# Optimization experiments

Hardware: AMD Instinct MI355X
Metric: run time of the kernel (lower is better)

## Reference

```python
import jax, jax.numpy as jnp
import numpy as np

N = 4096  # flattened_input_shape


def setup_inputs() -> dict:
    key = jax.random.key(0)
    ks = jax.random.split(key, 5)
    eps = 0.1
    center = jax.random.normal(ks[0], (1, N), dtype=jnp.float32)
    lb0 = center - eps  # initial interval lower bounds [1, N]
    ub0 = center + eps  # initial interval upper bounds [1, N]
    W1 = jax.random.normal(ks[1], (N, N), dtype=jnp.float32) / np.float32(np.sqrt(N))
    b1 = jax.random.normal(ks[2], (1, N), dtype=jnp.float32)
    W2 = jax.random.normal(ks[3], (N, N), dtype=jnp.float32) / np.float32(np.sqrt(N))
    b2 = jax.random.normal(ks[4], (1, N), dtype=jnp.float32)
    raw_alpha = jnp.ones((N,), dtype=jnp.float32)  # nn.Parameter init
    return {"raw_alpha": raw_alpha, "lb0": lb0, "ub0": ub0,
            "W1": W1, "b1": b1, "W2": W2, "b2": b2}


def _pos(x):
    return jnp.where(x > 0, x, jnp.zeros_like(x))


def _neg(x):
    return jnp.where(x < 0, x, jnp.zeros_like(x))


def _forward(raw_alpha, lb0, ub0, W1, b1, W2, b2):
    # ---- previous.backsubstitution(): compose affine2 over affine1 ----
    clslope, clintercept = W2, b2
    cuslope, cuintercept = W2, b2
    clp, cln = _pos(clslope), _neg(clslope)
    cup, cun = _pos(cuslope), _neg(cuslope)
    clintercept = b1 @ clp.T + b1 @ cln.T + clintercept  # [1, N]
    cuintercept = b1 @ cup.T + b1 @ cun.T + cuintercept  # [1, N]
    clslope = clp @ W1 + cln @ W1  # [N, N]
    cuslope = cup @ W1 + cun @ W1  # [N, N]
    # ---- certifier against initial interval bounds ----
    lbounds = lb0 @ _pos(clslope).T + ub0 @ _neg(clslope).T + clintercept  # [1, N]
    ubounds = ub0 @ _pos(cuslope).T + lb0 @ _neg(cuslope).T + cuintercept  # [1, N]
    # ---- DeepPolyReLU transformer ----
    alpha = jax.nn.sigmoid(raw_alpha)  # [N]
    lb = lbounds.reshape(-1)
    ub = ubounds.reshape(-1)
    denom = ub - lb
    # ub/(ub-lb) with NaN (0/0) replaced by 0, grad-safe
    relu_slope = jnp.where(denom == 0, 0.0, ub / jnp.where(denom == 0, 1.0, denom))  # [N]
    relu_intercept = (1.0 - relu_slope)[None, :] * ubounds  # [1, N]
    below = ub <= 0
    above = lb >= 0
    crossing = ~(below | above)
    base = jnp.where(above, 1.0, 0.0)  # [N]
    uslope = jnp.where(crossing, relu_slope, base)
    uintercept = jnp.where(crossing[None, :], relu_intercept, jnp.zeros((1, N), dtype=ubounds.dtype))
    lslope_v1 = jnp.where(crossing, 0.0, base)
    lslope_v2 = jnp.where(crossing, 1.0, base)
    lslope = alpha * lslope_v1 + (1.0 - alpha) * lslope_v2  # [N]
    lintercept = jnp.zeros((1, N), dtype=lbounds.dtype)
    return jnp.diag(lslope), lintercept, jnp.diag(uslope), uintercept


def reference(raw_alpha, lb0, ub0, W1, b1, W2, b2):
    return _forward(raw_alpha, lb0, ub0, W1, b1, W2, b2)
```

## Files before the change

### kernel.cpp

```cpp
#include <hip/hip_runtime.h>
#include <stdint.h>

#define N 4096
#define BM 128
#define BN 128
#define BK 128

#define TILE_BYTES 524288
#define KT_BYTES   16384

#define QSCALE 256.0f
#define INV_QQ (1.0f / 65536.0f)

typedef int v8i __attribute__((ext_vector_type(8)));
typedef float f32x16 __attribute__((ext_vector_type(16)));

union V8 { v8i v; uint4 h[2]; };

__device__ __forceinline__ void gload16(const unsigned char* g, unsigned char* l) {
  __builtin_amdgcn_global_load_lds(
      (const __attribute__((address_space(1))) unsigned int*)g,
      (__attribute__((address_space(3))) unsigned int*)l, 16, 0, 0);
}

__device__ __forceinline__ int pack4_fp8(float a, float b, float c, float d) {
  int r = __builtin_amdgcn_cvt_pk_fp8_f32(a, b, 0, false);
  r = __builtin_amdgcn_cvt_pk_fp8_f32(c, d, r, true);
  return r;
}

__global__ __launch_bounds__(256) void prep_w1(const float* __restrict__ W1,
                                               const float* __restrict__ lb0,
                                               const float* __restrict__ ub0,
                                               unsigned char* __restrict__ W1T,
                                               float* __restrict__ tvec) {
  __shared__ float tile[64 * 65];
  __shared__ float tdot[64];
  const int t = threadIdx.x;
  const int j0 = blockIdx.x * 64, k0 = blockIdx.y * 64;
  if (t < 64) tdot[t] = 0.f;
  __syncthreads();
#pragma unroll
  for (int s = 0; s < 4; ++s) {
    int ck = s * 256 + t;
    int row = ck >> 4;
    int col = (ck & 15) * 4;
    float4 v = *(const float4*)(W1 + (size_t)(k0 + row) * N + j0 + col);
    float4 l = *(const float4*)(lb0 + j0 + col);
    float4 u = *(const float4*)(ub0 + j0 + col);
    float part = v.x * 0.5f * (l.x + u.x) + v.y * 0.5f * (l.y + u.y)
               + v.z * 0.5f * (l.z + u.z) + v.w * 0.5f * (l.w + u.w);
    atomicAdd(&tdot[row], part);
    float* d = &tile[row * 65 + col];
    d[0] = v.x; d[1] = v.y; d[2] = v.z; d[3] = v.w;
  }
  __syncthreads();
  if (t < 64) atomicAdd(&tvec[k0 + t], tdot[t]);
  int jl = t >> 2, ch = (t & 3) * 16;
  float f[16];
#pragma unroll
  for (int m = 0; m < 16; ++m) f[m] = tile[(ch + m) * 65 + jl] * QSCALE;
  uint4 o;
  o.x = (unsigned)pack4_fp8(f[0], f[1], f[2], f[3]);
  o.y = (unsigned)pack4_fp8(f[4], f[5], f[6], f[7]);
  o.z = (unsigned)pack4_fp8(f[8], f[9], f[10], f[11]);
  o.w = (unsigned)pack4_fp8(f[12], f[13], f[14], f[15]);
  int j = j0 + jl;
  int kb = k0 + ch;
  *(uint4*)(W1T + (size_t)(j >> 7) * TILE_BYTES + (size_t)(kb >> 7) * KT_BYTES
            + (size_t)((kb >> 4) & 7) * 2048 + (j & 127) * 16) = o;
}

__global__ __launch_bounds__(256) void convert_w2(const float* __restrict__ W2,
                                                  const float* __restrict__ b1,
                                                  const float* __restrict__ tvec,
                                                  unsigned char* __restrict__ W2q,
                                                  float* __restrict__ cvec,
                                                  float* __restrict__ Sc) {
  const int t = threadIdx.x;
  const int i0 = blockIdx.y * 128;
  const int k0 = blockIdx.x * 128;
  const int r = t & 127;
  const int h = t >> 7;
  unsigned char* panel = W2q + (size_t)blockIdx.y * TILE_BYTES
                       + (size_t)blockIdx.x * KT_BYTES;
  float dotb = 0.f, dott = 0.f;
#pragma unroll
  for (int q = 0; q < 4; ++q) {
    int c = 2 * q + h;
    const float* p = W2 + (size_t)(i0 + r) * N + k0 + c * 16;
    alignas(16) int packed[4];
#pragma unroll
    for (int m = 0; m < 4; ++m) {
      float4 w = *(const float4*)(p + m * 4);
      float4 b = *(const float4*)(b1 + k0 + c * 16 + m * 4);
      float4 tv = *(const float4*)(tvec + k0 + c * 16 + m * 4);
      dotb += w.x * b.x + w.y * b.y + w.z * b.z + w.w * b.w;
      dott += w.x * tv.x + w.y * tv.y + w.z * tv.z + w.w * tv.w;
      packed[m] = pack4_fp8(w.x * QSCALE, w.y * QSCALE, w.z * QSCALE, w.w * QSCALE);
    }
    *(uint4*)(panel + (size_t)c * 2048 + r * 16) = *(const uint4*)packed;
  }
  __shared__ float redb[256], redt[256];
  redb[t] = dotb;
  redt[t] = dott;
  __syncthreads();
  if (t < 128) {
    float vb = redb[t] + redb[t + 128];
    float vt = redt[t] + redt[t + 128];
    atomicAdd(&cvec[i0 + t], vb);
    atomicAdd(&Sc[i0 + t], vt);
  }
}

__global__ __launch_bounds__(256, 4) void gemm_absrow(const unsigned char* __restrict__ A,
                                                      const unsigned char* __restrict__ B,
                                                      const float* __restrict__ lb0,
                                                      const float* __restrict__ ub0,
                                                      float* __restrict__ R_acc) {
  __shared__ __align__(16) unsigned char As[BM * BK];
  __shared__ __align__(16) unsigned char Bs[BN * BK];
  const int t = threadIdx.x;
  const int lane = t & 63, w = t >> 6;
  const int wm = (w >> 1) * 64, wn = (w & 1) * 64;
  const int i0 = blockIdx.y * BM, j0 = blockIdx.x * BN;
  const int l31 = lane & 31, half = lane >> 5;

  f32x16 acc[2][2] = {};
  const int sc1 = 0x7F7F7F7F;

  const unsigned char* ga = A + (size_t)blockIdx.y * TILE_BYTES + t * 16;
  const unsigned char* gb = B + (size_t)blockIdx.x * TILE_BYTES + t * 16;

  for (int kt = 0; kt < N / BK; ++kt) {
    __syncthreads();
#pragma unroll
    for (int p = 0; p < 4; ++p) {
      gload16(ga + p * 4096, &As[(p * 256 + t) * 16]);
      gload16(gb + p * 4096, &Bs[(p * 256 + t) * 16]);
    }
    __syncthreads();
#pragma unroll
    for (int h = 0; h < 2; ++h) {
      const int c0 = h * 4 + half * 2;
      V8 af[2], bfr[2];
#pragma unroll
      for (int tm = 0; tm < 2; ++tm) {
        const unsigned char* p = &As[c0 * 2048 + (wm + tm * 32 + l31) * 16];
        af[tm].h[0] = *(const uint4*)p;
        af[tm].h[1] = *(const uint4*)(p + 2048);
      }
#pragma unroll
      for (int tn = 0; tn < 2; ++tn) {
        const unsigned char* p = &Bs[c0 * 2048 + (wn + tn * 32 + l31) * 16];
        bfr[tn].h[0] = *(const uint4*)p;
        bfr[tn].h[1] = *(const uint4*)(p + 2048);
      }
#pragma unroll
      for (int tm = 0; tm < 2; ++tm)
#pragma unroll
        for (int tn = 0; tn < 2; ++tn)
          acc[tm][tn] = __builtin_amdgcn_mfma_scale_f32_32x32x64_f8f6f4(
              af[tm].v, bfr[tn].v, acc[tm][tn],
              0 , 0 ,
              0, sc1, 0, sc1);
    }
    ga += KT_BYTES;
    gb += KT_BYTES;
  }

  float epsv[2];
#pragma unroll
  for (int tn = 0; tn < 2; ++tn) {
    int j = j0 + wn + tn * 32 + l31;
    epsv[tn] = 0.5f * (ub0[j] - lb0[j]);
  }
#pragma unroll
  for (int tm = 0; tm < 2; ++tm) {
#pragma unroll
    for (int r = 0; r < 16; ++r) {
      float s = fabsf(acc[tm][0][r]) * epsv[0] + fabsf(acc[tm][1][r]) * epsv[1];
#pragma unroll
      for (int off = 1; off < 32; off <<= 1)
        s += __shfl_xor(s, off, 64);
      if (l31 == 0) {
        int i = i0 + wm + tm * 32 + (r & 3) + 8 * (r >> 2) + 4 * half;
        atomicAdd(&R_acc[i], s);
      }
    }
  }
}

struct ReluVals { float lslope, uslope, uinter; };

__device__ __forceinline__ ReluVals relu_vals(int i,
                                              const float* __restrict__ cvec,
                                              const float* __restrict__ Sc,
                                              const float* __restrict__ b2,
                                              const float* __restrict__ R_acc,
                                              const float* __restrict__ raw_alpha) {
  float mid = Sc[i] + cvec[i] + b2[i];
  float rr = R_acc[i] * INV_QQ;
  float lb = mid - rr;
  float ub = mid + rr;
  float alpha = 1.f / (1.f + expf(-raw_alpha[i]));
  float denom = ub - lb;
  float slope = (denom == 0.f) ? 0.f : ub / denom;
  bool below = ub <= 0.f, above = lb >= 0.f;
  bool crossing = !(below || above);
  float base = above ? 1.f : 0.f;
  ReluVals v;
  v.uslope = crossing ? slope : base;
  v.uinter = crossing ? (1.f - slope) * ub : 0.f;
  float l1 = crossing ? 0.f : base;
  float l2 = crossing ? 1.f : base;
  v.lslope = alpha * l1 + (1.f - alpha) * l2;
  return v;
}

__global__ __launch_bounds__(256) void fill_patch(float4* __restrict__ out, int n4,
                                                  const float* __restrict__ cvec,
                                                  const float* __restrict__ Sc,
                                                  const float* __restrict__ b2,
                                                  const float* __restrict__ R_acc,
                                                  const float* __restrict__ raw_alpha) {
  const size_t NN = (size_t)N * N;
  const size_t d1_end = NN;
  const size_t d2_beg = NN + N;
  const size_t d2_end = 2 * NN + N;
  int idx = blockIdx.x * 256 + threadIdx.x;
  int stride = gridDim.x * 256;
  for (int i = idx; i < n4; i += stride) {
    size_t e = 4 * (size_t)i;
    float4 v = make_float4(0.f, 0.f, 0.f, 0.f);
    if (e >= d2_end) {
      int b = (int)(e - d2_end);
      v.x = relu_vals(b + 0, cvec, Sc, b2, R_acc, raw_alpha).uinter;
      v.y = relu_vals(b + 1, cvec, Sc, b2, R_acc, raw_alpha).uinter;
      v.z = relu_vals(b + 2, cvec, Sc, b2, R_acc, raw_alpha).uinter;
      v.w = relu_vals(b + 3, cvec, Sc, b2, R_acc, raw_alpha).uinter;
    } else if (e < d1_end) {
      int r = (int)(e >> 12), c = (int)(e & 4095);
      if (r >= c && r < c + 4)
        (&v.x)[r - c] = relu_vals(r, cvec, Sc, b2, R_acc, raw_alpha).lslope;
    } else if (e >= d2_beg) {
      size_t e2 = e - d2_beg;
      int r = (int)(e2 >> 12), c = (int)(e2 & 4095);
      if (r >= c && r < c + 4)
        (&v.x)[r - c] = relu_vals(r, cvec, Sc, b2, R_acc, raw_alpha).uslope;
    }
    out[i] = v;
  }
}

extern "C" void kernel_launch(void* const* d_in, const int* in_sizes, int n_in,
                              void* d_out, int out_size, void* d_ws, size_t ws_size,
                              hipStream_t stream) {
  const float* raw_alpha = (const float*)d_in[0];
  const float* lb0 = (const float*)d_in[1];
  const float* ub0 = (const float*)d_in[2];
  const float* W1 = (const float*)d_in[3];
  const float* b1 = (const float*)d_in[4];
  const float* W2 = (const float*)d_in[5];
  const float* b2 = (const float*)d_in[6];

  float* tvec = (float*)d_ws;
  float* cvec = tvec + N;
  float* Sc = cvec + N;
  float* R_acc = Sc + N;

  unsigned char* W2q = (unsigned char*)d_out;
  unsigned char* W1Tq = W2q + (size_t)N * N;

  (void)hipMemsetAsync(d_ws, 0, 4 * N * sizeof(float), stream);
  prep_w1<<<dim3(N / 64, N / 64), 256, 0, stream>>>(W1, lb0, ub0, W1Tq, tvec);
  convert_w2<<<dim3(N / 128, N / 128), 256, 0, stream>>>(W2, b1, tvec, W2q, cvec, Sc);
  gemm_absrow<<<dim3(N / BN, N / BM), 256, 0, stream>>>(W2q, W1Tq, lb0, ub0, R_acc);
  int n4 = out_size / 4;
  fill_patch<<<8192, 256, 0, stream>>>((float4*)d_out, n4, cvec, Sc, b2, R_acc, raw_alpha);
}
```

Before: 359.6 us.

## Enlarge GEMM tiles to 256x256 with double-buffered async LDS pipeline

The FP8 GEMM moves from 128x128 tiles with 256 threads to 256x256 tiles with 512 threads, so each wave computes a 128x64 sub-block. LDS is double-buffered, and global-to-LDS loads for the next k-step are issued before computing the current one, using vmcnt waits in place of full syncthreads. It also adds block-index swizzling for L2 locality and s_setprio around the MFMA bursts. Separately, prep_w1 swaps its LDS atomic row reduction for wave shuffles. The larger tiles cut global traffic but raise register and LDS use, and the hand-written waitcnt logic has to be exactly right to stay correct.

```diff
diff --git a/kernel.cpp b/kernel.cpp
--- a/kernel.cpp
+++ b/kernel.cpp
@@ -2,9 +2,6 @@
 #include <stdint.h>
 
 #define N 4096
-#define BM 128
-#define BN 128
-#define BK 128
 
 #define TILE_BYTES 524288
 #define KT_BYTES   16384
@@ -38,8 +35,6 @@
   __shared__ float tdot[64];
   const int t = threadIdx.x;
   const int j0 = blockIdx.x * 64, k0 = blockIdx.y * 64;
-  if (t < 64) tdot[t] = 0.f;
-  __syncthreads();
 #pragma unroll
   for (int s = 0; s < 4; ++s) {
     int ck = s * 256 + t;
@@ -50,7 +45,11 @@
     float4 u = *(const float4*)(ub0 + j0 + col);
     float part = v.x * 0.5f * (l.x + u.x) + v.y * 0.5f * (l.y + u.y)
                + v.z * 0.5f * (l.z + u.z) + v.w * 0.5f * (l.w + u.w);
-    atomicAdd(&tdot[row], part);
+    part += __shfl_xor(part, 1, 64);
+    part += __shfl_xor(part, 2, 64);
+    part += __shfl_xor(part, 4, 64);
+    part += __shfl_xor(part, 8, 64);
+    if ((t & 15) == 0) tdot[row] = part;
     float* d = &tile[row * 65 + col];
     d[0] = v.x; d[1] = v.y; d[2] = v.z; d[3] = v.w;
   }
@@ -113,70 +112,101 @@
   }
 }
 
-__global__ __launch_bounds__(256, 4) void gemm_absrow(const unsigned char* __restrict__ A,
+#define NT 32
+__global__ __launch_bounds__(512, 2) void gemm_absrow(const unsigned char* __restrict__ A,
                                                       const unsigned char* __restrict__ B,
                                                       const float* __restrict__ lb0,
                                                       const float* __restrict__ ub0,
                                                       float* __restrict__ R_acc) {
-  __shared__ __align__(16) unsigned char As[BM * BK];
-  __shared__ __align__(16) unsigned char Bs[BN * BK];
+  __shared__ __align__(16) unsigned char sm[4 * 32768];
   const int t = threadIdx.x;
   const int lane = t & 63, w = t >> 6;
-  const int wm = (w >> 1) * 64, wn = (w & 1) * 64;
-  const int i0 = blockIdx.y * BM, j0 = blockIdx.x * BN;
+  const int wr = w >> 2, wc = w & 3;
   const int l31 = lane & 31, half = lane >> 5;
 
-  f32x16 acc[2][2] = {};
+  const int bid = blockIdx.y * 16 + blockIdx.x;
+  const int swz = (bid & 7) * 32 + (bid >> 3);
+  const int bm = swz >> 4, bn = swz & 15;
+  const int i0 = bm * 256, j0 = bn * 256;
+
+  const unsigned char* gA0 = A + (size_t)(2 * bm) * TILE_BYTES + t * 16;
+  const unsigned char* gA1 = gA0 + TILE_BYTES;
+  const unsigned char* gB0 = B + (size_t)(2 * bn) * TILE_BYTES + t * 16;
+  const unsigned char* gB1 = gB0 + TILE_BYTES;
+
+  f32x16 acc[4][2] = {};
   const int sc1 = 0x7F7F7F7F;
 
-  const unsigned char* ga = A + (size_t)blockIdx.y * TILE_BYTES + t * 16;
-  const unsigned char* gb = B + (size_t)blockIdx.x * TILE_BYTES + t * 16;
-
-  for (int kt = 0; kt < N / BK; ++kt) {
-    __syncthreads();
-#pragma unroll
-    for (int p = 0; p < 4; ++p) {
-      gload16(ga + p * 4096, &As[(p * 256 + t) * 16]);
-      gload16(gb + p * 4096, &Bs[(p * 256 + t) * 16]);
-    }
-    __syncthreads();
+  auto stage = [&](int kt, int h) {
+    const int g = ((kt & 1) << 1) | h;
+    unsigned char* d = sm + g * 32768 + t * 16;
+    const size_t off = (size_t)kt * KT_BYTES + (size_t)h * 8192;
+    gload16(gA0 + off, d);
+    gload16(gA1 + off, d + 8192);
+    gload16(gB0 + off, d + 16384);
+    gload16(gB1 + off, d + 24576);
+  };
+
+  auto compute = [&](int kt, int h) {
+    const unsigned char* base = sm + (((kt & 1) << 1) | h) * 32768;
+    V8 af[4], bf[2];
+    const unsigned char* pa = base + wr * 8192 + (half * 2) * 2048 + l31 * 16;
+#pragma unroll
+    for (int tm = 0; tm < 4; ++tm) {
+      const unsigned char* p = pa + tm * 512;
+      af[tm].h[0] = *(const uint4*)p;
+      af[tm].h[1] = *(const uint4*)(p + 2048);
+    }
+#pragma unroll
+    for (int tn = 0; tn < 2; ++tn) {
+      const int j = wc * 64 + tn * 32 + l31;
+      const unsigned char* p = base + 16384 + (j >> 7) * 8192
+                             + (half * 2) * 2048 + (j & 127) * 16;
+      bf[tn].h[0] = *(const uint4*)p;
+      bf[tn].h[1] = *(const uint4*)(p + 2048);
+    }
+    __builtin_amdgcn_s_setprio(1);
+#pragma unroll
+    for (int tm = 0; tm < 4; ++tm)
+#pragma unroll
+      for (int tn = 0; tn < 2; ++tn)
+        acc[tm][tn] = __builtin_amdgcn_mfma_scale_f32_32x32x64_f8f6f4(
+            af[tm].v, bf[tn].v, acc[tm][tn],
+            0 , 0 ,
+            0, sc1, 0, sc1);
+    __builtin_amdgcn_s_setprio(0);
+  };
+
+  stage(0, 0);
+  stage(0, 1);
+
+  for (int kt = 0; kt < NT - 1; ++kt) {
 #pragma unroll
     for (int h = 0; h < 2; ++h) {
-      const int c0 = h * 4 + half * 2;
-      V8 af[2], bfr[2];
-#pragma unroll
-      for (int tm = 0; tm < 2; ++tm) {
-        const unsigned char* p = &As[c0 * 2048 + (wm + tm * 32 + l31) * 16];
-        af[tm].h[0] = *(const uint4*)p;
-        af[tm].h[1] = *(const uint4*)(p + 2048);
-      }
-#pragma unroll
-      for (int tn = 0; tn < 2; ++tn) {
-        const unsigned char* p = &Bs[c0 * 2048 + (wn + tn * 32 + l31) * 16];
-        bfr[tn].h[0] = *(const uint4*)p;
-        bfr[tn].h[1] = *(const uint4*)(p + 2048);
-      }
-#pragma unroll
-      for (int tm = 0; tm < 2; ++tm)
-#pragma unroll
-        for (int tn = 0; tn < 2; ++tn)
-          acc[tm][tn] = __builtin_amdgcn_mfma_scale_f32_32x32x64_f8f6f4(
-              af[tm].v, bfr[tn].v, acc[tm][tn],
-              0 , 0 ,
-              0, sc1, 0, sc1);
-    }
-    ga += KT_BYTES;
-    gb += KT_BYTES;
-  }
+      stage(kt + 1, h);
+      asm volatile("s_waitcnt vmcnt(8)" ::: "memory");
+      __builtin_amdgcn_s_barrier();
+      asm volatile("" ::: "memory");
+      compute(kt, h);
+    }
+  }
+  asm volatile("s_waitcnt vmcnt(4)" ::: "memory");
+  __builtin_amdgcn_s_barrier();
+  asm volatile("" ::: "memory");
+  compute(NT - 1, 0);
+  asm volatile("s_waitcnt vmcnt(0)" ::: "memory");
+  __builtin_amdgcn_s_barrier();
+  asm volatile("" ::: "memory");
+  compute(NT - 1, 1);
 
   float epsv[2];
 #pragma unroll
   for (int tn = 0; tn < 2; ++tn) {
-    int j = j0 + wn + tn * 32 + l31;
+    int j = j0 + wc * 64 + tn * 32 + l31;
     epsv[tn] = 0.5f * (ub0[j] - lb0[j]);
   }
 #pragma unroll
-  for (int tm = 0; tm < 2; ++tm) {
+  for (int tm = 0; tm < 4; ++tm) {
 #pragma unroll
     for (int r = 0; r < 16; ++r) {
       float s = fabsf(acc[tm][0][r]) * epsv[0] + fabsf(acc[tm][1][r]) * epsv[1];
@@ -184,7 +214,7 @@
       for (int off = 1; off < 32; off <<= 1)
         s += __shfl_xor(s, off, 64);
       if (l31 == 0) {
-        int i = i0 + wm + tm * 32 + (r & 3) + 8 * (r >> 2) + 4 * half;
+        int i = i0 + wr * 128 + tm * 32 + (r & 3) + 8 * (r >> 2) + 4 * half;
         atomicAdd(&R_acc[i], s);
       }
     }
@@ -275,7 +305,7 @@
   (void)hipMemsetAsync(d_ws, 0, 4 * N * sizeof(float), stream);
   prep_w1<<<dim3(N / 64, N / 64), 256, 0, stream>>>(W1, lb0, ub0, W1Tq, tvec);
   convert_w2<<<dim3(N / 128, N / 128), 256, 0, stream>>>(W2, b1, tvec, W2q, cvec, Sc);
-  gemm_absrow<<<dim3(N / BN, N / BM), 256, 0, stream>>>(W2q, W1Tq, lb0, ub0, R_acc);
+  gemm_absrow<<<dim3(16, 16), 512, 0, stream>>>(W2q, W1Tq, lb0, ub0, R_acc);
   int n4 = out_size / 4;
   fill_patch<<<8192, 256, 0, stream>>>((float4*)d_out, n4, cvec, Sc, b2, R_acc, raw_alpha);
 }
```

After: 357.2 us. Within noise of the previous version (-0.7%).
